# Performance work log

Measured on AMD Instinct MI355X. Metric: run time of the kernel, lower is better.

The kernel has to match this reference:

```python
import jax, jax.numpy as jnp
import numpy as np

B, T, D, H, K = 2, 1024, 1024, 4096, 8


def setup_inputs() -> dict:
    key = jax.random.key(0)
    ks = jax.random.split(key, 5)
    x = jax.random.normal(ks[0], (B, T, D), dtype=jnp.float32)
    # hard one-hot routing weights per token (no learned router)
    expert_ids = jax.random.randint(ks[1], (B, T), 0, K)
    combine_weights = jax.nn.one_hot(expert_ids, K, dtype=jnp.float32)
    scale_in = 1.0 / np.sqrt(D)
    scale_h = 1.0 / np.sqrt(H)
    wg = jax.random.normal(ks[2], (K, D, H), dtype=jnp.float32) * scale_in
    wu = jax.random.normal(ks[3], (K, D, H), dtype=jnp.float32) * scale_in
    wd = jax.random.normal(ks[4], (K, H, D), dtype=jnp.float32) * scale_h
    return {"x": x, "combine_weights": combine_weights, "wg": wg, "wu": wu, "wd": wd}


def reference(x, combine_weights, wg, wu, wd):
    # Each expert is a SwiGLU FFN: down( silu(gate(x)) * up(x) ).
    # Dense baseline: every token runs through all K experts (as in source).
    g = jnp.einsum('btd,kdh->btkh', x, wg)          # [B,T,K,H]
    u = jnp.einsum('btd,kdh->btkh', x, wu)          # [B,T,K,H]
    h = jax.nn.silu(g) * u                          # [B,T,K,H]
    expert_outs = jnp.einsum('btkh,khd->btkd', h, wd)  # [B,T,K,D]
    y = jnp.einsum('btk,btkd->btd', combine_weights, expert_outs)
    return y.astype(x.dtype)
```

## Files before the change

kernel.cpp:

```cpp
#include <hip/hip_runtime.h>

typedef __attribute__((ext_vector_type(8))) short bf16x8;
typedef __attribute__((ext_vector_type(4))) float f32x4;
typedef unsigned short u16;

#define NTOK 2048
#define DDIM 1024
#define HDIM 4096
#define KEXP 8

#define BM 320
#define BK 64
#define NDESC 16

__device__ __forceinline__ u16 f2bf(float f) {
  union { float f; unsigned int u; } c; c.f = f;
  unsigned int u = c.u;
  return (u16)((u + 0x7FFFu + ((u >> 16) & 1u)) >> 16);
}
__device__ __forceinline__ unsigned pk2(float a, float b) {
  return (unsigned)f2bf(a) | ((unsigned)f2bf(b) << 16);
}

#define BAR() do { \
  asm volatile("s_waitcnt lgkmcnt(0)" ::: "memory"); \
  __builtin_amdgcn_sched_barrier(0); \
  __builtin_amdgcn_s_barrier(); \
  __builtin_amdgcn_sched_barrier(0); \
} while (0)

__global__ void route_kernel(const float* __restrict__ cw, int* __restrict__ offs,
                             int* __restrict__ perm, float* __restrict__ wsel,
                             int* __restrict__ desc) {
  __shared__ int cnt[KEXP];
  __shared__ int base[KEXP];
  const int t = threadIdx.x;
  if (t < KEXP) cnt[t] = 0;
  __syncthreads();
  int eid[8]; float wv[8];
  #pragma unroll
  for (int i = 0; i < 8; i++) {
    const int tok = t * 8 + i;
    const float* p = cw + tok * KEXP;
    int best = 0; float bw = p[0];
    #pragma unroll
    for (int k = 1; k < KEXP; k++) { float v = p[k]; if (v > bw) { bw = v; best = k; } }
    eid[i] = best; wv[i] = bw;
    atomicAdd(&cnt[best], 1);
  }
  __syncthreads();
  if (t == 0) {
    int s = 0, nd = 0;
    for (int k = 0; k < KEXP; k++) {
      const int ck = cnt[k];
      base[k] = s; offs[k] = s;
      for (int m0 = 0; m0 < ck && nd < NDESC; m0 += BM)
        desc[nd++] = (k << 12) | (s + m0);
      s += ck;
    }
    offs[KEXP] = s;
    for (; nd < NDESC; nd++) desc[nd] = -1;
  }
  __syncthreads();
  #pragma unroll
  for (int i = 0; i < 8; i++) {
    const int tok = t * 8 + i;
    const int pos = atomicAdd(&base[eid[i]], 1);
    perm[pos] = tok;
    wsel[pos] = wv[i];
  }
}

__global__ void gather_x(const float* __restrict__ x, const int* __restrict__ perm,
                         u16* __restrict__ Xb) {
  const int slot = blockIdx.x;
  const int tok = perm[slot];
  const int t = threadIdx.x;
  float4 v = ((const float4*)(x + (size_t)tok * DDIM))[t];
  ushort4 o; o.x = f2bf(v.x); o.y = f2bf(v.y); o.z = f2bf(v.z); o.w = f2bf(v.w);
  ((ushort4*)(Xb + (size_t)slot * DDIM))[t] = o;
}

__global__ __launch_bounds__(1024, 4) void gemm_swiglu(
    const u16* __restrict__ Xb,
    const float* __restrict__ wg, const float* __restrict__ wu,
    const int* __restrict__ offs, const int* __restrict__ desc,
    u16* __restrict__ Hb) {
  __shared__ u16 As[2][BM * 64];
  __shared__ u16 Bs[2][2][64 * 64];

  const int d = desc[blockIdx.y];
  if (d < 0) return;
  const int e = d >> 12;
  const int slot0 = d & 0xFFF;
  const int Msub = offs[e + 1] - slot0;
  const int n0 = blockIdx.x * 64;

  const int t = threadIdx.x;
  const int lane = t & 63;
  const int W = t >> 6;
  const int wm = W >> 2;
  const int wn = W & 3;
  const int l15 = lane & 15;
  const int lhi = lane >> 4;

  const bool do_a = t < 640;
  const int a_row = t >> 1;
  const int a_c0 = (t & 1) * 4;
  const u16* a_src = Xb + (size_t)min(slot0 + a_row, NTOK - 1) * DDIM + a_c0 * 8;
  const int a_swz = a_row & 7;

  const int tb = t & 511;
  const int matsel = t >> 9;
  const float* b_base = (matsel ? wu : wg) + (size_t)e * DDIM * HDIM;
  const int b_n = tb & 63;
  const int b_c = tb >> 6;
  const float* b_src = b_base + (size_t)(b_c * 8) * HDIM + n0 + b_n;
  const int b_off = b_n * 64 + ((b_c ^ (b_n & 7)) << 3);

  float bR[8];
  uint4 aT0, aT1, aT2, aT3;
  f32x4 accg[5] = {};
  f32x4 accu[5] = {};

  #define AISSUE(tile) if (do_a) { const uint4* p_ = (const uint4*)(a_src + (tile) * BK); \
    aT0 = p_[0]; aT1 = p_[1]; aT2 = p_[2]; aT3 = p_[3]; }
  #define AWRITE(buf) if (do_a) { u16* base_ = &As[buf][a_row * 64]; \
    *(uint4*)(base_ + (((a_c0 + 0) ^ a_swz) << 3)) = aT0; \
    *(uint4*)(base_ + (((a_c0 + 1) ^ a_swz) << 3)) = aT1; \
    *(uint4*)(base_ + (((a_c0 + 2) ^ a_swz) << 3)) = aT2; \
    *(uint4*)(base_ + (((a_c0 + 3) ^ a_swz) << 3)) = aT3; }
  #define LOADB(tile) { const float* p_ = b_src + (size_t)(tile) * BK * HDIM; \
    _Pragma("unroll") for (int j = 0; j < 8; j++) bR[j] = p_[(size_t)j * HDIM]; }
  #define WRITEB(buf) { uint4 w_; \
    w_.x = pk2(bR[0], bR[1]); w_.y = pk2(bR[2], bR[3]); \
    w_.z = pk2(bR[4], bR[5]); w_.w = pk2(bR[6], bR[7]); \
    *(uint4*)(&Bs[buf][matsel][b_off]) = w_; }
  #define COMPUTE(buf) { _Pragma("unroll") for (int ks = 0; ks < 2; ks++) { \
      const int cx_ = (((ks << 2) + lhi) ^ (l15 & 7)) << 3; \
      bf16x8 bg_ = *(const bf16x8*)(&Bs[buf][0][(wn * 16 + l15) * 64] + cx_); \
      bf16x8 bu_ = *(const bf16x8*)(&Bs[buf][1][(wn * 16 + l15) * 64] + cx_); \
      _Pragma("unroll") for (int fm = 0; fm < 5; fm++) { \
        bf16x8 af_ = *(const bf16x8*)(&As[buf][(wm * 80 + fm * 16 + l15) * 64] + cx_); \
        accg[fm] = __builtin_amdgcn_mfma_f32_16x16x32_bf16(af_, bg_, accg[fm], 0, 0, 0); \
        accu[fm] = __builtin_amdgcn_mfma_f32_16x16x32_bf16(af_, bu_, accu[fm], 0, 0, 0); } } }

  LOADB(0);
  AISSUE(0);
  WRITEB(0);
  LOADB(1);
  AWRITE(0);
  BAR();

  #pragma unroll 1
  for (int it = 0; it < 16; it += 2) {
    if (it + 1 < 16) AISSUE(it + 1);
    __builtin_amdgcn_sched_barrier(0);
    COMPUTE(0);
    if (it + 1 < 16) {
      WRITEB(1);
      if (it + 2 < 16) LOADB(it + 2);
      AWRITE(1);
    }
    BAR();
    if (it + 2 < 16) AISSUE(it + 2);
    __builtin_amdgcn_sched_barrier(0);
    COMPUTE(1);
    if (it + 2 < 16) {
      WRITEB(0);
      if (it + 3 < 16) LOADB(it + 3);
      AWRITE(0);
    }
    BAR();
  }
  #undef AISSUE
  #undef AWRITE
  #undef LOADB
  #undef WRITEB
  #undef COMPUTE

  #pragma unroll
  for (int fm = 0; fm < 5; fm++) {
    #pragma unroll
    for (int i = 0; i < 4; i++) {
      const int row = wm * 80 + fm * 16 + lhi * 4 + i;
      if (row < Msub) {
        const float g = accg[fm][i];
        const float u = accu[fm][i];
        const float h = (g / (1.0f + __expf(-g))) * u;
        Hb[(size_t)(slot0 + row) * HDIM + n0 + wn * 16 + l15] = f2bf(h);
      }
    }
  }
}

__global__ __launch_bounds__(1024, 4) void gemm_down(
    const u16* __restrict__ Hb, const float* __restrict__ wd,
    const int* __restrict__ offs, const int* __restrict__ desc,
    const int* __restrict__ perm, const float* __restrict__ wsel,
    float* __restrict__ y) {
  __shared__ u16 As[2][BM * 64];
  __shared__ u16 Bs[2][128 * 64];

  const int d = desc[blockIdx.y];
  if (d < 0) return;
  const int e = d >> 12;
  const int slot0 = d & 0xFFF;
  const int Msub = offs[e + 1] - slot0;
  const int n0 = blockIdx.x * 128;
  const int kbase = blockIdx.z * (HDIM / 4);

  const float* Wd = wd + (size_t)e * HDIM * DDIM;

  const int t = threadIdx.x;
  const int lane = t & 63;
  const int W = t >> 6;
  const int wm = W >> 2;
  const int wn = W & 3;
  const int l15 = lane & 15;
  const int lhi = lane >> 4;

  const bool do_a = t < 640;
  const int a_row = t >> 1;
  const int a_c0 = (t & 1) * 4;
  const u16* a_src = Hb + (size_t)min(slot0 + a_row, NTOK - 1) * HDIM + kbase + a_c0 * 8;
  const int a_swz = a_row & 7;

  const int b_n = t & 127;
  const int b_c = t >> 7;
  const float* b_src = Wd + (size_t)(kbase + b_c * 8) * DDIM + n0 + b_n;
  const int b_off = b_n * 64 + ((b_c ^ (b_n & 7)) << 3);

  float bR[8];
  uint4 aT0, aT1, aT2, aT3;
  f32x4 acc[5][2] = {};

  #define AISSUE(tile) if (do_a) { const uint4* p_ = (const uint4*)(a_src + (tile) * BK); \
    aT0 = p_[0]; aT1 = p_[1]; aT2 = p_[2]; aT3 = p_[3]; }
  #define AWRITE(buf) if (do_a) { u16* base_ = &As[buf][a_row * 64]; \
    *(uint4*)(base_ + (((a_c0 + 0) ^ a_swz) << 3)) = aT0; \
    *(uint4*)(base_ + (((a_c0 + 1) ^ a_swz) << 3)) = aT1; \
    *(uint4*)(base_ + (((a_c0 + 2) ^ a_swz) << 3)) = aT2; \
    *(uint4*)(base_ + (((a_c0 + 3) ^ a_swz) << 3)) = aT3; }
  #define LOADB(tile) { const float* p_ = b_src + (size_t)(tile) * BK * DDIM; \
    _Pragma("unroll") for (int j = 0; j < 8; j++) bR[j] = p_[(size_t)j * DDIM]; }
  #define WRITEB(buf) { uint4 w_; \
    w_.x = pk2(bR[0], bR[1]); w_.y = pk2(bR[2], bR[3]); \
    w_.z = pk2(bR[4], bR[5]); w_.w = pk2(bR[6], bR[7]); \
    *(uint4*)(&Bs[buf][b_off]) = w_; }
  #define COMPUTE(buf) { _Pragma("unroll") for (int ks = 0; ks < 2; ks++) { \
      const int cx_ = (((ks << 2) + lhi) ^ (l15 & 7)) << 3; \
      bf16x8 bf0_ = *(const bf16x8*)(&Bs[buf][(wn * 32 + l15) * 64] + cx_); \
      bf16x8 bf1_ = *(const bf16x8*)(&Bs[buf][(wn * 32 + 16 + l15) * 64] + cx_); \
      _Pragma("unroll") for (int fm = 0; fm < 5; fm++) { \
        bf16x8 af_ = *(const bf16x8*)(&As[buf][(wm * 80 + fm * 16 + l15) * 64] + cx_); \
        acc[fm][0] = __builtin_amdgcn_mfma_f32_16x16x32_bf16(af_, bf0_, acc[fm][0], 0, 0, 0); \
        acc[fm][1] = __builtin_amdgcn_mfma_f32_16x16x32_bf16(af_, bf1_, acc[fm][1], 0, 0, 0); } } }

  LOADB(0);
  AISSUE(0);
  WRITEB(0);
  LOADB(1);
  AWRITE(0);
  BAR();

  #pragma unroll 1
  for (int it = 0; it < 16; it += 2) {
    if (it + 1 < 16) AISSUE(it + 1);
    __builtin_amdgcn_sched_barrier(0);
    COMPUTE(0);
    if (it + 1 < 16) {
      WRITEB(1);
      if (it + 2 < 16) LOADB(it + 2);
      AWRITE(1);
    }
    BAR();
    if (it + 2 < 16) AISSUE(it + 2);
    __builtin_amdgcn_sched_barrier(0);
    COMPUTE(1);
    if (it + 2 < 16) {
      WRITEB(0);
      if (it + 3 < 16) LOADB(it + 3);
      AWRITE(0);
    }
    BAR();
  }
  #undef AISSUE
  #undef AWRITE
  #undef LOADB
  #undef WRITEB
  #undef COMPUTE

  #pragma unroll
  for (int fm = 0; fm < 5; fm++) {
    #pragma unroll
    for (int i = 0; i < 4; i++) {
      const int row = wm * 80 + fm * 16 + lhi * 4 + i;
      if (row < Msub) {
        const int slot = slot0 + row;
        const int tok = perm[slot];
        const float w = wsel[slot];
        const size_t base = (size_t)tok * DDIM + n0 + wn * 32;
        atomicAdd(y + base + l15, acc[fm][0][i] * w);
        atomicAdd(y + base + 16 + l15, acc[fm][1][i] * w);
      }
    }
  }
}

extern "C" void kernel_launch(void* const* d_in, const int* in_sizes, int n_in,
                              void* d_out, int out_size, void* d_ws, size_t ws_size,
                              hipStream_t stream) {
  const float* x  = (const float*)d_in[0];
  const float* cw = (const float*)d_in[1];
  const float* wg = (const float*)d_in[2];
  const float* wu = (const float*)d_in[3];
  const float* wd = (const float*)d_in[4];
  float* y = (float*)d_out;

  char* ws = (char*)d_ws;
  int* offs   = (int*)ws;
  int* desc   = (int*)(ws + 64);
  int* perm   = (int*)(ws + 128);
  float* wsel = (float*)(ws + 128 + NTOK * 4);
  u16* Xb = (u16*)(ws + 32768);
  u16* Hb = (u16*)(ws + 32768 + (size_t)NTOK * DDIM * 2);

  hipMemsetAsync(d_out, 0, (size_t)NTOK * DDIM * sizeof(float), stream);
  route_kernel<<<1, 256, 0, stream>>>(cw, offs, perm, wsel, desc);
  gather_x<<<NTOK, 256, 0, stream>>>(x, perm, Xb);
  gemm_swiglu<<<dim3(HDIM / 64, NDESC), 1024, 0, stream>>>(Xb, wg, wu, offs, desc, Hb);
  gemm_down<<<dim3(DDIM / 128, NDESC, 4), 1024, 0, stream>>>(Hb, wd, offs, desc, perm, wsel, y);
}
```

Before: 154.2 us.

## Split fused gate/up GEMM into separate GEMMs plus standalone SwiGLU kernel

The fused gate+up GEMM becomes a generic GEMM launched with a z-dimension selecting gate or up weights, each block covering 128 columns of one matrix. A separate elementwise kernel then applies SiLU(g)*u over bf16 intermediates, writing in place into the gate buffer. This gives each block a wider tile of a single matrix and more blocks. In exchange it adds a kernel launch, extra global round trips for two NTOK×HDIM bf16 buffers, and rounds g and u to bf16 before the activation. The bf16 conversion now uses the HIP library routine.

```diff
diff --git a/kernel.cpp b/kernel.cpp
--- a/kernel.cpp
+++ b/kernel.cpp
@@ -1,4 +1,5 @@
 #include <hip/hip_runtime.h>
+#include <hip/hip_bf16.h>
 
 typedef __attribute__((ext_vector_type(8))) short bf16x8;
 typedef __attribute__((ext_vector_type(4))) float f32x4;
@@ -14,12 +15,14 @@
 #define NDESC 16
 
 __device__ __forceinline__ u16 f2bf(float f) {
-  union { float f; unsigned int u; } c; c.f = f;
-  unsigned int u = c.u;
-  return (u16)((u + 0x7FFFu + ((u >> 16) & 1u)) >> 16);
+  __hip_bfloat16 b = __float2bfloat16(f);
+  union { __hip_bfloat16 b; u16 u; } c; c.b = b; return c.u;
 }
 __device__ __forceinline__ unsigned pk2(float a, float b) {
   return (unsigned)f2bf(a) | ((unsigned)f2bf(b) << 16);
+}
+__device__ __forceinline__ float bf2f(unsigned hi16) {
+  union { unsigned u; float f; } c; c.u = hi16; return c.f;
 }
 
 #define BAR() do { \
@@ -81,20 +84,24 @@
   ((ushort4*)(Xb + (size_t)slot * DDIM))[t] = o;
 }
 
-__global__ __launch_bounds__(1024, 4) void gemm_swiglu(
+__global__ __launch_bounds__(1024, 4) void gemm_nt(
     const u16* __restrict__ Xb,
     const float* __restrict__ wg, const float* __restrict__ wu,
     const int* __restrict__ offs, const int* __restrict__ desc,
-    u16* __restrict__ Hb) {
+    u16* __restrict__ Gb, u16* __restrict__ Ub) {
   __shared__ u16 As[2][BM * 64];
-  __shared__ u16 Bs[2][2][64 * 64];
+  __shared__ u16 Bs[2][128 * 64];
 
   const int d = desc[blockIdx.y];
   if (d < 0) return;
   const int e = d >> 12;
   const int slot0 = d & 0xFFF;
   const int Msub = offs[e + 1] - slot0;
-  const int n0 = blockIdx.x * 64;
+  const int n0 = blockIdx.x * 128;
+  const int mat = blockIdx.z;
+
+  const float* Wsrc = (mat ? wu : wg) + (size_t)e * DDIM * HDIM;
+  u16* Out = mat ? Ub : Gb;
 
   const int t = threadIdx.x;
   const int lane = t & 63;
@@ -110,18 +117,14 @@
   const u16* a_src = Xb + (size_t)min(slot0 + a_row, NTOK - 1) * DDIM + a_c0 * 8;
   const int a_swz = a_row & 7;
 
-  const int tb = t & 511;
-  const int matsel = t >> 9;
-  const float* b_base = (matsel ? wu : wg) + (size_t)e * DDIM * HDIM;
-  const int b_n = tb & 63;
-  const int b_c = tb >> 6;
-  const float* b_src = b_base + (size_t)(b_c * 8) * HDIM + n0 + b_n;
+  const int b_n = t & 127;
+  const int b_c = t >> 7;
+  const float* b_src = Wsrc + (size_t)(b_c * 8) * HDIM + n0 + b_n;
   const int b_off = b_n * 64 + ((b_c ^ (b_n & 7)) << 3);
 
   float bR[8];
   uint4 aT0, aT1, aT2, aT3;
-  f32x4 accg[5] = {};
-  f32x4 accu[5] = {};
+  f32x4 acc[5][2] = {};
 
   #define AISSUE(tile) if (do_a) { const uint4* p_ = (const uint4*)(a_src + (tile) * BK); \
     aT0 = p_[0]; aT1 = p_[1]; aT2 = p_[2]; aT3 = p_[3]; }
@@ -135,15 +138,15 @@
   #define WRITEB(buf) { uint4 w_; \
     w_.x = pk2(bR[0], bR[1]); w_.y = pk2(bR[2], bR[3]); \
     w_.z = pk2(bR[4], bR[5]); w_.w = pk2(bR[6], bR[7]); \
-    *(uint4*)(&Bs[buf][matsel][b_off]) = w_; }
+    *(uint4*)(&Bs[buf][b_off]) = w_; }
   #define COMPUTE(buf) { _Pragma("unroll") for (int ks = 0; ks < 2; ks++) { \
       const int cx_ = (((ks << 2) + lhi) ^ (l15 & 7)) << 3; \
-      bf16x8 bg_ = *(const bf16x8*)(&Bs[buf][0][(wn * 16 + l15) * 64] + cx_); \
-      bf16x8 bu_ = *(const bf16x8*)(&Bs[buf][1][(wn * 16 + l15) * 64] + cx_); \
+      bf16x8 bf0_ = *(const bf16x8*)(&Bs[buf][(wn * 32 + l15) * 64] + cx_); \
+      bf16x8 bf1_ = *(const bf16x8*)(&Bs[buf][(wn * 32 + 16 + l15) * 64] + cx_); \
       _Pragma("unroll") for (int fm = 0; fm < 5; fm++) { \
         bf16x8 af_ = *(const bf16x8*)(&As[buf][(wm * 80 + fm * 16 + l15) * 64] + cx_); \
-        accg[fm] = __builtin_amdgcn_mfma_f32_16x16x32_bf16(af_, bg_, accg[fm], 0, 0, 0); \
-        accu[fm] = __builtin_amdgcn_mfma_f32_16x16x32_bf16(af_, bu_, accu[fm], 0, 0, 0); } } }
+        acc[fm][0] = __builtin_amdgcn_mfma_f32_16x16x32_bf16(af_, bf0_, acc[fm][0], 0, 0, 0); \
+        acc[fm][1] = __builtin_amdgcn_mfma_f32_16x16x32_bf16(af_, bf1_, acc[fm][1], 0, 0, 0); } } }
 
   LOADB(0);
   AISSUE(0);
@@ -185,13 +188,31 @@
     for (int i = 0; i < 4; i++) {
       const int row = wm * 80 + fm * 16 + lhi * 4 + i;
       if (row < Msub) {
-        const float g = accg[fm][i];
-        const float u = accu[fm][i];
-        const float h = (g / (1.0f + __expf(-g))) * u;
-        Hb[(size_t)(slot0 + row) * HDIM + n0 + wn * 16 + l15] = f2bf(h);
+        const size_t base = (size_t)(slot0 + row) * HDIM + n0 + wn * 32;
+        Out[base + l15] = f2bf(acc[fm][0][i]);
+        Out[base + 16 + l15] = f2bf(acc[fm][1][i]);
       }
     }
   }
+}
+
+__global__ void swiglu_combine(u16* __restrict__ Gb, const u16* __restrict__ Ub) {
+  const size_t i = ((size_t)blockIdx.x * 256 + threadIdx.x) * 8;
+  uint4 gv = *(const uint4*)(Gb + i);
+  uint4 uv = *(const uint4*)(Ub + i);
+  const unsigned* gp = (const unsigned*)&gv;
+  const unsigned* up = (const unsigned*)&uv;
+  uint4 ov;
+  unsigned* op = (unsigned*)&ov;
+  #pragma unroll
+  for (int j = 0; j < 4; j++) {
+    const float g0 = bf2f(gp[j] << 16), g1 = bf2f(gp[j] & 0xFFFF0000u);
+    const float u0 = bf2f(up[j] << 16), u1 = bf2f(up[j] & 0xFFFF0000u);
+    const float h0 = (g0 / (1.0f + __expf(-g0))) * u0;
+    const float h1 = (g1 / (1.0f + __expf(-g1))) * u1;
+    op[j] = pk2(h0, h1);
+  }
+  *(uint4*)(Gb + i) = ov;
 }
 
 __global__ __launch_bounds__(1024, 4) void gemm_down(
@@ -324,11 +345,14 @@
   int* perm   = (int*)(ws + 128);
   float* wsel = (float*)(ws + 128 + NTOK * 4);
   u16* Xb = (u16*)(ws + 32768);
-  u16* Hb = (u16*)(ws + 32768 + (size_t)NTOK * DDIM * 2);
+  u16* Gb = (u16*)(ws + 32768 + (size_t)NTOK * DDIM * 2);
+  u16* Ub = (u16*)(ws + 32768 + (size_t)NTOK * DDIM * 2
+                          + (size_t)NTOK * HDIM * 2);
 
   hipMemsetAsync(d_out, 0, (size_t)NTOK * DDIM * sizeof(float), stream);
   route_kernel<<<1, 256, 0, stream>>>(cw, offs, perm, wsel, desc);
   gather_x<<<NTOK, 256, 0, stream>>>(x, perm, Xb);
-  gemm_swiglu<<<dim3(HDIM / 64, NDESC), 1024, 0, stream>>>(Xb, wg, wu, offs, desc, Hb);
-  gemm_down<<<dim3(DDIM / 128, NDESC, 4), 1024, 0, stream>>>(Hb, wd, offs, desc, perm, wsel, y);
-}
+  gemm_nt<<<dim3(HDIM / 128, NDESC, 2), 1024, 0, stream>>>(Xb, wg, wu, offs, desc, Gb, Ub);
+  swiglu_combine<<<(NTOK * HDIM / 8) / 256, 256, 0, stream>>>(Gb, Ub);
+  gemm_down<<<dim3(DDIM / 128, NDESC, 4), 1024, 0, stream>>>(Gb, wd, offs, desc, perm, wsel, y);
+}
```

Result: slower. 160.1 us (+3.8%).

## Shrink swiglu GEMM tile to 32 columns with 512 threads and single-buffered A

Applied to the files above, without the earlier changes.

The gate/up GEMM now uses 32-wide N tiles with 512-thread blocks, doubling the grid. The A tile is single-buffered and loaded synchronously each iteration. This drops the software-pipelined A prefetch and adds an extra barrier per step, in exchange for lower LDS use and more, smaller blocks per CU. The bf16 conversion also switches to the HIP intrinsic. The trade-offs are that each block rereads the X tile for half as many columns, doubling A traffic, and that global-load latency on A is no longer hidden.

```diff
diff --git a/kernel.cpp b/kernel.cpp
--- a/kernel.cpp
+++ b/kernel.cpp
@@ -1,4 +1,5 @@
 #include <hip/hip_runtime.h>
+#include <hip/hip_bf16.h>
 
 typedef __attribute__((ext_vector_type(8))) short bf16x8;
 typedef __attribute__((ext_vector_type(4))) float f32x4;
@@ -14,9 +15,8 @@
 #define NDESC 16
 
 __device__ __forceinline__ u16 f2bf(float f) {
-  union { float f; unsigned int u; } c; c.f = f;
-  unsigned int u = c.u;
-  return (u16)((u + 0x7FFFu + ((u >> 16) & 1u)) >> 16);
+  __hip_bfloat16 b = __float2bfloat16(f);
+  union { __hip_bfloat16 b; u16 u; } c; c.b = b; return c.u;
 }
 __device__ __forceinline__ unsigned pk2(float a, float b) {
   return (unsigned)f2bf(a) | ((unsigned)f2bf(b) << 16);
@@ -81,55 +81,66 @@
   ((ushort4*)(Xb + (size_t)slot * DDIM))[t] = o;
 }
 
-__global__ __launch_bounds__(1024, 4) void gemm_swiglu(
+__global__ __launch_bounds__(512, 4) void gemm_swiglu(
     const u16* __restrict__ Xb,
     const float* __restrict__ wg, const float* __restrict__ wu,
     const int* __restrict__ offs, const int* __restrict__ desc,
     u16* __restrict__ Hb) {
-  __shared__ u16 As[2][BM * 64];
-  __shared__ u16 Bs[2][2][64 * 64];
+  __shared__ u16 As[BM * 64];
+  __shared__ u16 Bs[2][2][32 * 64];
 
   const int d = desc[blockIdx.y];
   if (d < 0) return;
   const int e = d >> 12;
   const int slot0 = d & 0xFFF;
   const int Msub = offs[e + 1] - slot0;
-  const int n0 = blockIdx.x * 64;
+  const int n0 = blockIdx.x * 32;
 
   const int t = threadIdx.x;
   const int lane = t & 63;
   const int W = t >> 6;
-  const int wm = W >> 2;
-  const int wn = W & 3;
+  const int wm = W >> 1;
+  const int wn = W & 1;
   const int l15 = lane & 15;
   const int lhi = lane >> 4;
 
-  const bool do_a = t < 640;
-  const int a_row = t >> 1;
-  const int a_c0 = (t & 1) * 4;
-  const u16* a_src = Xb + (size_t)min(slot0 + a_row, NTOK - 1) * DDIM + a_c0 * 8;
-  const int a_swz = a_row & 7;
-
-  const int tb = t & 511;
-  const int matsel = t >> 9;
+  const int a_row1 = t >> 1;
+  const int a_h1 = (t & 1) * 4;
+  const u16* a_src1 = Xb + (size_t)min(slot0 + a_row1, NTOK - 1) * DDIM + a_h1 * 8;
+  const int a_sz1 = a_row1 & 7;
+  const int a_row2 = 256 + (t >> 1);
+  const u16* a_src2 = Xb + (size_t)min(slot0 + a_row2, NTOK - 1) * DDIM + a_h1 * 8;
+  const int a_sz2 = a_row2 & 7;
+  const bool do_a2 = t < 128;
+
+  const int tb = t & 255;
+  const int matsel = t >> 8;
   const float* b_base = (matsel ? wu : wg) + (size_t)e * DDIM * HDIM;
-  const int b_n = tb & 63;
-  const int b_c = tb >> 6;
+  const int b_n = tb & 31;
+  const int b_c = tb >> 5;
   const float* b_src = b_base + (size_t)(b_c * 8) * HDIM + n0 + b_n;
   const int b_off = b_n * 64 + ((b_c ^ (b_n & 7)) << 3);
 
   float bR[8];
-  uint4 aT0, aT1, aT2, aT3;
   f32x4 accg[5] = {};
   f32x4 accu[5] = {};
 
-  #define AISSUE(tile) if (do_a) { const uint4* p_ = (const uint4*)(a_src + (tile) * BK); \
-    aT0 = p_[0]; aT1 = p_[1]; aT2 = p_[2]; aT3 = p_[3]; }
-  #define AWRITE(buf) if (do_a) { u16* base_ = &As[buf][a_row * 64]; \
-    *(uint4*)(base_ + (((a_c0 + 0) ^ a_swz) << 3)) = aT0; \
-    *(uint4*)(base_ + (((a_c0 + 1) ^ a_swz) << 3)) = aT1; \
-    *(uint4*)(base_ + (((a_c0 + 2) ^ a_swz) << 3)) = aT2; \
-    *(uint4*)(base_ + (((a_c0 + 3) ^ a_swz) << 3)) = aT3; }
+  #define ASTAGE(tile) { \
+    { const uint4* p_ = (const uint4*)(a_src1 + (tile) * BK); \
+      uint4 v0_ = p_[0], v1_ = p_[1], v2_ = p_[2], v3_ = p_[3]; \
+      u16* b_ = &As[a_row1 * 64]; \
+      *(uint4*)(b_ + (((a_h1 + 0) ^ a_sz1) << 3)) = v0_; \
+      *(uint4*)(b_ + (((a_h1 + 1) ^ a_sz1) << 3)) = v1_; \
+      *(uint4*)(b_ + (((a_h1 + 2) ^ a_sz1) << 3)) = v2_; \
+      *(uint4*)(b_ + (((a_h1 + 3) ^ a_sz1) << 3)) = v3_; } \
+    if (do_a2) { const uint4* p_ = (const uint4*)(a_src2 + (tile) * BK); \
+      uint4 v0_ = p_[0], v1_ = p_[1], v2_ = p_[2], v3_ = p_[3]; \
+      u16* b_ = &As[a_row2 * 64]; \
+      *(uint4*)(b_ + (((a_h1 + 0) ^ a_sz2) << 3)) = v0_; \
+      *(uint4*)(b_ + (((a_h1 + 1) ^ a_sz2) << 3)) = v1_; \
+      *(uint4*)(b_ + (((a_h1 + 2) ^ a_sz2) << 3)) = v2_; \
+      *(uint4*)(b_ + (((a_h1 + 3) ^ a_sz2) << 3)) = v3_; } \
+  }
   #define LOADB(tile) { const float* p_ = b_src + (size_t)(tile) * BK * HDIM; \
     _Pragma("unroll") for (int j = 0; j < 8; j++) bR[j] = p_[(size_t)j * HDIM]; }
   #define WRITEB(buf) { uint4 w_; \
@@ -141,40 +152,23 @@
       bf16x8 bg_ = *(const bf16x8*)(&Bs[buf][0][(wn * 16 + l15) * 64] + cx_); \
       bf16x8 bu_ = *(const bf16x8*)(&Bs[buf][1][(wn * 16 + l15) * 64] + cx_); \
       _Pragma("unroll") for (int fm = 0; fm < 5; fm++) { \
-        bf16x8 af_ = *(const bf16x8*)(&As[buf][(wm * 80 + fm * 16 + l15) * 64] + cx_); \
+        bf16x8 af_ = *(const bf16x8*)(&As[(wm * 80 + fm * 16 + l15) * 64] + cx_); \
         accg[fm] = __builtin_amdgcn_mfma_f32_16x16x32_bf16(af_, bg_, accg[fm], 0, 0, 0); \
         accu[fm] = __builtin_amdgcn_mfma_f32_16x16x32_bf16(af_, bu_, accu[fm], 0, 0, 0); } } }
 
   LOADB(0);
-  AISSUE(0);
-  WRITEB(0);
-  LOADB(1);
-  AWRITE(0);
-  BAR();
 
   #pragma unroll 1
-  for (int it = 0; it < 16; it += 2) {
-    if (it + 1 < 16) AISSUE(it + 1);
-    __builtin_amdgcn_sched_barrier(0);
-    COMPUTE(0);
-    if (it + 1 < 16) {
-      WRITEB(1);
-      if (it + 2 < 16) LOADB(it + 2);
-      AWRITE(1);
-    }
+  for (int it = 0; it < 16; ++it) {
+    const int buf = it & 1;
+    if (it) __syncthreads();
+    ASTAGE(it);
+    WRITEB(buf);
+    if (it + 1 < 16) LOADB(it + 1);
     BAR();
-    if (it + 2 < 16) AISSUE(it + 2);
-    __builtin_amdgcn_sched_barrier(0);
-    COMPUTE(1);
-    if (it + 2 < 16) {
-      WRITEB(0);
-      if (it + 3 < 16) LOADB(it + 3);
-      AWRITE(0);
-    }
-    BAR();
-  }
-  #undef AISSUE
-  #undef AWRITE
+    COMPUTE(buf);
+  }
+  #undef ASTAGE
   #undef LOADB
   #undef WRITEB
   #undef COMPUTE
@@ -329,6 +323,6 @@
   hipMemsetAsync(d_out, 0, (size_t)NTOK * DDIM * sizeof(float), stream);
   route_kernel<<<1, 256, 0, stream>>>(cw, offs, perm, wsel, desc);
   gather_x<<<NTOK, 256, 0, stream>>>(x, perm, Xb);
-  gemm_swiglu<<<dim3(HDIM / 64, NDESC), 1024, 0, stream>>>(Xb, wg, wu, offs, desc, Hb);
+  gemm_swiglu<<<dim3(HDIM / 32, NDESC), 512, 0, stream>>>(Xb, wg, wu, offs, desc, Hb);
   gemm_down<<<dim3(DDIM / 128, NDESC, 4), 1024, 0, stream>>>(Hb, wd, offs, desc, perm, wsel, y);
 }
```

Result: slower. 177.1 us (+14.8%).
